# Kernel tuning notes

Measured on AMD Instinct MI355X. Metric: run time of the kernel, lower is better.

Reference implementation:

```python
import jax, jax.numpy as jnp
import numpy as np

B, S, D = 2, 2048, 1024
H = 16
HD = D // H  # 64


def setup_inputs() -> dict:
    key = jax.random.key(0)
    ks = jax.random.split(key, 6)
    sc = 1.0 / np.sqrt(D)
    x = jax.random.normal(ks[0], (B, S, D), dtype=jnp.float32)
    Wq = jax.random.normal(ks[1], (D, D), dtype=jnp.float32) * sc
    Wk = jax.random.normal(ks[2], (D, D), dtype=jnp.float32) * sc
    Wv = jax.random.normal(ks[3], (D, D), dtype=jnp.float32) * sc
    Wo = jax.random.normal(ks[4], (D, D), dtype=jnp.float32) * sc
    bo = jax.random.normal(ks[5], (D,), dtype=jnp.float32) * 0.01
    return {"x": x, "Wq": Wq, "Wk": Wk, "Wv": Wv, "Wo": Wo, "bo": bo}


def reference(x, Wq, Wk, Wv, Wo, bo):
    # projections: [B,S,D] -> [B,H,S,HD]
    def split_heads(t):
        return t.reshape(B, S, H, HD).transpose(0, 2, 1, 3)

    q = split_heads(x @ Wq)
    k = split_heads(x @ Wk)
    v = split_heads(x @ Wv)

    # naive full score matrix [B,H,S,S], masked causal, scaled softmax
    scores = jnp.einsum("bhqd,bhkd->bhqk", q, k)
    causal = jnp.tril(jnp.ones((S, S), dtype=bool))  # True = keep
    scores = jnp.where(causal, scores, -jnp.inf)
    attn = jax.nn.softmax(scores / np.sqrt(HD), axis=-1)

    ctx = jnp.einsum("bhqk,bhkd->bhqd", attn, v)  # [B,H,S,HD]
    ctx = ctx.transpose(0, 2, 1, 3).reshape(B, S, D)
    return ctx @ Wo + bo
```

## Files before the change

### kernel.cpp

```cpp
#include <hip/hip_runtime.h>

#define BB 2
#define SS 2048
#define DD 1024
#define HH 16
#define HD 64
#define MM (BB*SS)

typedef __bf16 bf16x8 __attribute__((ext_vector_type(8)));
typedef short  s16x4  __attribute__((ext_vector_type(4)));
typedef float  f32x4  __attribute__((ext_vector_type(4)));

#ifndef __has_builtin
#define __has_builtin(x) 0
#endif

__device__ __forceinline__ unsigned short f2bf(float f) {
    unsigned int u = __float_as_uint(f);
    u = (u + 0x7fffu + ((u >> 16) & 1u)) >> 16;
    return (unsigned short)u;
}
__device__ __forceinline__ unsigned int pack2(float a, float b) {
    return (unsigned int)f2bf(a) | ((unsigned int)f2bf(b) << 16);
}
__device__ __forceinline__ unsigned int pack2_fast(float a, float b) {
#if __has_builtin(__builtin_amdgcn_perm)
    return __builtin_amdgcn_perm(__float_as_uint(b) + 0x8000u,
                                 __float_as_uint(a) + 0x8000u, 0x07060302u);
#else
    return ((__float_as_uint(a) + 0x8000u) >> 16) |
           ((__float_as_uint(b) + 0x8000u) & 0xffff0000u);
#endif
}

__device__ __forceinline__ void gload_lds16(const unsigned short* g, unsigned short* l) {
    __builtin_amdgcn_global_load_lds(
        (const __attribute__((address_space(1))) void*)g,
        (__attribute__((address_space(3))) void*)l, 16, 0, 0);
}

__global__ __launch_bounds__(256) void prep_kernel(const float* __restrict__ x,
                                                   const float* __restrict__ Wq,
                                                   const float* __restrict__ Wk,
                                                   const float* __restrict__ Wv,
                                                   const float* __restrict__ Wo,
                                                   unsigned short* __restrict__ Xb,
                                                   unsigned short* __restrict__ Wqkvt,
                                                   unsigned short* __restrict__ Wot) {
    __shared__ float tile[32][33];
    const int bx = blockIdx.x;
    const int t = threadIdx.x;
    if (bx < 2048) {
        int gid = bx * 256 + t;
        int i = gid * 8;
        float4 a = *(const float4*)(x + i);
        float4 b = *(const float4*)(x + i + 4);
        uint4 o;
        o.x = pack2(a.x, a.y); o.y = pack2(a.z, a.w);
        o.z = pack2(b.x, b.y); o.w = pack2(b.z, b.w);
        ((uint4*)Xb)[gid] = o;
        return;
    }
    int pb = bx - 2048;
    int p = pb >> 10, rem = pb & 1023;
    int bxx = rem & 31, byy = rem >> 5;
    const float* src = (p == 0) ? Wq : (p == 1) ? Wk : (p == 2) ? Wv : Wo;
    unsigned short* dst = (p == 3) ? Wot : (Wqkvt + (size_t)p * DD * DD);
    int tx = t & 31, ty = t >> 5;
    int n = bxx * 32 + tx;
#pragma unroll
    for (int i = 0; i < 4; ++i) {
        int k = byy * 32 + ty + i * 8;
        tile[ty + i * 8][tx] = src[k * DD + n];
    }
    __syncthreads();
#pragma unroll
    for (int i = 0; i < 4; ++i) {
        int n2 = bxx * 32 + ty + i * 8;
        int k2 = byy * 32 + tx;
        dst[n2 * DD + k2] = f2bf(tile[tx][ty + i * 8]);
    }
}

#define GEMM_K_LOOP(Aglob, Bglob)                                                 \
    __shared__ unsigned short smem[128 * 132];                                    \
    unsigned short (*As)[64]  = (unsigned short(*)[64])smem;                      \
    unsigned short (*Bs)[64]  = (unsigned short(*)[64])(smem + 128 * 64);         \
    unsigned short (*Es)[132] = (unsigned short(*)[132])smem;                     \
    const int n0 = blockIdx.x * 128, m0 = blockIdx.y * 128;                       \
    const int t = threadIdx.x;                                                    \
    const int wave = t >> 6, lane = t & 63;                                       \
    const int wm = wave >> 1, wn = wave & 1;                                      \
    const int l15 = lane & 15, quad = lane >> 4;                                  \
    const int lr = lane >> 3, lg = (lane & 7);                                    \
    const int lc = (lg ^ lr) * 8;                    \
    f32x4 acc[4][4];                                                              \
    _Pragma("unroll") for (int i = 0; i < 4; ++i)                                 \
        _Pragma("unroll") for (int j = 0; j < 4; ++j) acc[i][j] = f32x4{0,0,0,0}; \
    for (int kt = 0; kt < 16; ++kt) {                                             \
        if (kt) __syncthreads();                                                  \
        _Pragma("unroll") for (int i = 0; i < 4; ++i) {                           \
            int row = wave * 32 + i * 8;                                          \
            gload_lds16(Aglob + (size_t)(m0 + row + lr) * DD + kt * 64 + lc, &As[row][0]); \
            gload_lds16(Bglob + (size_t)(n0 + row + lr) * DD + kt * 64 + lc, &Bs[row][0]); \
        }                                                                         \
        __syncthreads();                                                          \
        _Pragma("unroll") for (int kh = 0; kh < 2; ++kh) {                        \
            bf16x8 af[4], bfr[4];                                                 \
            _Pragma("unroll") for (int s = 0; s < 4; ++s)                         \
                af[s] = *(const bf16x8*)&As[wm * 64 + s * 16 + l15][((kh * 4 + quad) ^ (l15 & 7)) * 8]; \
            _Pragma("unroll") for (int s = 0; s < 4; ++s)                         \
                bfr[s] = *(const bf16x8*)&Bs[wn * 64 + s * 16 + l15][((kh * 4 + quad) ^ (l15 & 7)) * 8]; \
            _Pragma("unroll") for (int i = 0; i < 4; ++i)                         \
                _Pragma("unroll") for (int j = 0; j < 4; ++j)                     \
                    acc[i][j] = __builtin_amdgcn_mfma_f32_16x16x32_bf16(af[i], bfr[j], acc[i][j], 0, 0, 0); \
        }                                                                         \
    }                                                                             \
    __syncthreads();

__global__ __launch_bounds__(256) void qkv_gemm_kernel(const unsigned short* __restrict__ Xb,
                                                       const unsigned short* __restrict__ Wt,
                                                       unsigned short* __restrict__ Qg,
                                                       unsigned short* __restrict__ Kg,
                                                       unsigned short* __restrict__ Vt) {
    GEMM_K_LOOP(Xb, Wt)
    const int p = n0 >> 10;
    const float qs = (p == 0) ? 0.18033688011112042f : 1.0f;
    if (p < 2) {
#pragma unroll
        for (int sm = 0; sm < 4; ++sm)
#pragma unroll
            for (int sn = 0; sn < 4; ++sn)
#pragma unroll
                for (int i = 0; i < 4; ++i)
                    Es[wm * 64 + sm * 16 + quad * 4 + i][wn * 64 + sn * 16 + l15] = f2bf(acc[sm][sn][i] * qs);
    } else {
#pragma unroll
        for (int sm = 0; sm < 4; ++sm)
#pragma unroll
            for (int sn = 0; sn < 4; ++sn)
#pragma unroll
                for (int i = 0; i < 4; ++i)
                    Es[wn * 64 + sn * 16 + l15][wm * 64 + sm * 16 + quad * 4 + i] = f2bf(acc[sm][sn][i]);
    }
    __syncthreads();
    const int h0 = (n0 & 1023) >> 6;
    if (p < 2) {
        unsigned short* dst0 = p ? Kg : Qg;
        int ml = t >> 1, seg = t & 1;
        int gm = m0 + ml, b = gm >> 11, s = gm & 2047;
        unsigned short* dptr = dst0 + ((size_t)(b * HH + h0 + seg) * SS + s) * HD;
#pragma unroll
        for (int j = 0; j < 8; ++j)
            *(uint4*)(dptr + j * 8) = *(const uint4*)&Es[ml][seg * 64 + j * 8];
    } else {
        int nl = t >> 1, mh = t & 1;
        int h = h0 + (nl >> 6), hd = nl & 63;
        int b = m0 >> 11, s0 = (m0 & 2047) + mh * 64;
        unsigned short* dptr = Vt + ((size_t)(b * HH + h) * HD + hd) * SS + s0;
#pragma unroll
        for (int j = 0; j < 8; ++j)
            *(uint4*)(dptr + j * 8) = *(const uint4*)&Es[nl][mh * 64 + j * 8];
    }
}

__global__ __launch_bounds__(256) void out_gemm_kernel(const unsigned short* __restrict__ Ctxb,
                                                       const unsigned short* __restrict__ Wot,
                                                       const float* __restrict__ bo,
                                                       float* __restrict__ out) {
    GEMM_K_LOOP(Ctxb, Wot)
    (void)Es;
#pragma unroll
    for (int sn = 0; sn < 4; ++sn) {
        int gn = n0 + wn * 64 + sn * 16 + l15;
        float bias = bo[gn];
#pragma unroll
        for (int sm = 0; sm < 4; ++sm)
#pragma unroll
            for (int i = 0; i < 4; ++i) {
                int gm = m0 + wm * 64 + sm * 16 + quad * 4 + i;
                out[(size_t)gm * DD + gn] = acc[sm][sn][i] + bias;
            }
    }
}

__global__ __launch_bounds__(256) void attn_kernel(const unsigned short* __restrict__ Qg,
                                                   const unsigned short* __restrict__ Kg,
                                                   const unsigned short* __restrict__ Vt,
                                                   unsigned short* __restrict__ Ctxb) {
    __shared__ unsigned short Ks[2][128][64];
    __shared__ unsigned short Vs[2][64][128];

    const int bh = blockIdx.x;
    const int pi = blockIdx.y;
    const int t = threadIdx.x;
    const int wave = t >> 6, lane = t & 63;
    const int l15 = lane & 15, quad = lane >> 4;
    const int q0A = pi * 64;
    const int q0B = (31 - pi) * 64;
    const int aIters = (pi + 2) >> 1;
    const int bIters = (33 - pi) >> 1;
    const int b = bh >> 4, h = bh & 15;

    const unsigned short* Qb = Qg + (size_t)bh * SS * HD;
    const unsigned short* Kb = Kg + (size_t)bh * SS * HD;
    const unsigned short* Vb = Vt + (size_t)bh * HD * SS;

    const int qrow0 = q0A + wave * 16 + l15;
    const int qrow1 = q0B + wave * 16 + l15;
    const int qA_hi = q0A + wave * 16 + 15;
    const int qB_hi = q0B + wave * 16 + 15;
    bf16x8 bq[2][2];
#pragma unroll
    for (int hh = 0; hh < 2; ++hh) {
        bq[0][hh] = *(const bf16x8*)(Qb + (size_t)qrow0 * HD + hh * 32 + quad * 8);
        bq[1][hh] = *(const bf16x8*)(Qb + (size_t)qrow1 * HD + hh * 32 + quad * 8);
    }

    const int rloc = lane >> 3, pcl = lane & 7;
    const int vrl = lane >> 4, vgc = lane & 15;
    const unsigned short* ksrc[4];
    const unsigned short* vsrc[4];
#pragma unroll
    for (int j = 0; j < 4; ++j) {
        int krow = (wave * 4 + j) * 8 + rloc;
        ksrc[j] = Kb + (size_t)krow * HD + (pcl ^ rloc) * 8;
        int vrow = wave * 16 + j * 4 + vrl;
        vsrc[j] = Vb + (size_t)vrow * SS + (vgc ^ (vrow & 15)) * 8;
    }

    f32x4 acc[2][4];
#pragma unroll
    for (int qf = 0; qf < 2; ++qf)
#pragma unroll
        for (int db = 0; db < 4; ++db) acc[qf][db] = f32x4{0,0,0,0};
    f32x4 accl[2] = {f32x4{0,0,0,0}, f32x4{0,0,0,0}};
    const s16x4 ones = {(short)0x3F80, (short)0x3F80, (short)0x3F80, (short)0x3F80};

#pragma unroll
    for (int j = 0; j < 4; ++j) {
        gload_lds16(ksrc[j], &Ks[0][(wave * 4 + j) * 8][0]);
        gload_lds16(vsrc[j], &Vs[0][wave * 16 + j * 4][0]);
    }
    __syncthreads();

    for (int kt = 0; kt < bIters; ++kt) {
        const int buf = kt & 1;
        const int k0 = kt * 128;
        if (kt + 1 < bIters) {
            const int nb = buf ^ 1;
#pragma unroll
            for (int j = 0; j < 4; ++j) {
                gload_lds16(ksrc[j] + (size_t)(kt + 1) * 128 * HD, &Ks[nb][(wave * 4 + j) * 8][0]);
                gload_lds16(vsrc[j] + (kt + 1) * 128,              &Vs[nb][wave * 16 + j * 4][0]);
            }
        }

        const bool diagA = (kt == aIters - 1);
        const bool diagB = (kt == bIters - 1);
        const bool inA = (kt < aIters);
#pragma unroll
        for (int kb = 0; kb < 8; ++kb) {
            const int kbase = k0 + kb * 16;
            const bool a0 = inA && (kbase <= qA_hi);
            const bool a1 = (kbase <= qB_hi);
            if (!a0 && !a1) continue;
            bf16x8 ak[2];
#pragma unroll
            for (int hh = 0; hh < 2; ++hh)
                ak[hh] = *(const bf16x8*)&Ks[buf][kb * 16 + l15][((hh * 4 + quad) ^ (l15 & 7)) * 8];

            f32x4 St[2] = {f32x4{0,0,0,0}, f32x4{0,0,0,0}};
            if (a0) {
#pragma unroll
                for (int hh = 0; hh < 2; ++hh)
                    St[0] = __builtin_amdgcn_mfma_f32_16x16x32_bf16(ak[hh], bq[0][hh], St[0], 0, 0, 0);
                if (diagA) {
#pragma unroll
                    for (int r = 0; r < 4; ++r)
                        if (kbase + quad * 4 + r > qrow0) St[0][r] = -1e30f;
                }
            }
            if (a1) {
#pragma unroll
                for (int hh = 0; hh < 2; ++hh)
                    St[1] = __builtin_amdgcn_mfma_f32_16x16x32_bf16(ak[hh], bq[1][hh], St[1], 0, 0, 0);
                if (diagB) {
#pragma unroll
                    for (int r = 0; r < 4; ++r)
                        if (kbase + quad * 4 + r > qrow1) St[1][r] = -1e30f;
                }
            }

            s16x4 ap[2];
#pragma unroll
            for (int qf = 0; qf < 2; ++qf) {
                float e0 = __builtin_amdgcn_exp2f(St[qf][0]);
                float e1 = __builtin_amdgcn_exp2f(St[qf][1]);
                float e2 = __builtin_amdgcn_exp2f(St[qf][2]);
                float e3 = __builtin_amdgcn_exp2f(St[qf][3]);
                uint2 uu;
                uu.x = pack2_fast(e0, e1);
                uu.y = pack2_fast(e2, e3);
                ap[qf] = *(s16x4*)&uu;
            }

#pragma unroll
            for (int db = 0; db < 4; ++db) {
                const int pg = (2 * kb + (quad >> 1)) ^ l15;
                s16x4 bv = *(const s16x4*)&Vs[buf][db * 16 + l15][pg * 8 + (quad & 1) * 4];
                if (a0) acc[0][db] = __builtin_amdgcn_mfma_f32_16x16x16bf16_1k(ap[0], bv, acc[0][db], 0, 0, 0);
                if (a1) acc[1][db] = __builtin_amdgcn_mfma_f32_16x16x16bf16_1k(ap[1], bv, acc[1][db], 0, 0, 0);
            }
            if (a0) accl[0] = __builtin_amdgcn_mfma_f32_16x16x16bf16_1k(ap[0], ones, accl[0], 0, 0, 0);
            if (a1) accl[1] = __builtin_amdgcn_mfma_f32_16x16x16bf16_1k(ap[1], ones, accl[1], 0, 0, 0);
        }

        __syncthreads();
    }

#pragma unroll
    for (int qf = 0; qf < 2; ++qf) {
        const int qb0 = (qf == 0) ? q0A : q0B;
#pragma unroll
        for (int r = 0; r < 4; ++r) {
            float ir = 1.0f / accl[qf][r];
            int gq = qb0 + wave * 16 + quad * 4 + r;
            size_t base = ((size_t)(b * SS + gq)) * DD + h * HD;
#pragma unroll
            for (int db = 0; db < 4; ++db)
                Ctxb[base + db * 16 + l15] = f2bf(acc[qf][db][r] * ir);
        }
    }
}

extern "C" void kernel_launch(void* const* d_in, const int* in_sizes, int n_in,
                              void* d_out, int out_size, void* d_ws, size_t ws_size,
                              hipStream_t stream) {
    const float* x  = (const float*)d_in[0];
    const float* Wq = (const float*)d_in[1];
    const float* Wk = (const float*)d_in[2];
    const float* Wv = (const float*)d_in[3];
    const float* Wo = (const float*)d_in[4];
    const float* bo = (const float*)d_in[5];
    float* out = (float*)d_out;

    char* w = (char*)d_ws;
    unsigned short* Xb    = (unsigned short*)(w);
    unsigned short* Wqkvt = (unsigned short*)(w + (size_t)(8 << 20));
    unsigned short* Wot   = (unsigned short*)(w + (size_t)(14 << 20));
    unsigned short* Qg    = (unsigned short*)(w + (size_t)(16 << 20));
    unsigned short* Kg    = (unsigned short*)(w + (size_t)(24 << 20));
    unsigned short* Vt    = (unsigned short*)(w + (size_t)(32 << 20));
    unsigned short* Ctxb  = (unsigned short*)(w + (size_t)(40 << 20));

    prep_kernel<<<6144, 256, 0, stream>>>(x, Wq, Wk, Wv, Wo, Xb, Wqkvt, Wot);
    qkv_gemm_kernel<<<dim3(3 * DD / 128, MM / 128), 256, 0, stream>>>(Xb, Wqkvt, Qg, Kg, Vt);
    attn_kernel<<<dim3(BB * HH, 16), 256, 0, stream>>>(Qg, Kg, Vt, Ctxb);
    out_gemm_kernel<<<dim3(DD / 128, MM / 128), 256, 0, stream>>>(Ctxb, Wot, bo, out);
}
```

Baseline: 207.2 us.

## Split causal attention loop into paired and tail phases; widen weight-transpose tiles

The attention kernel's single key-tile loop, which evaluated per-16-key predicates for both query blocks, becomes two loops. The first covers tiles both query blocks need and runs unconditionally, masking only the diagonal. The second covers only the long query block's remaining tiles, removing branch and predicate overhead from the inner MFMA loop. The prep kernel's weight transpose moves from 32x32 to 64x64 tiles with 16-byte packed bf16 stores and half the blocks, trading possible LDS bank conflicts on the strided reads for fewer, wider global writes.

Result: faster. 174.8 us (-15.6%).

```diff
diff --git a/kernel.cpp b/kernel.cpp
--- a/kernel.cpp
+++ b/kernel.cpp
@@ -47,7 +47,7 @@
                                                    unsigned short* __restrict__ Xb,
                                                    unsigned short* __restrict__ Wqkvt,
                                                    unsigned short* __restrict__ Wot) {
-    __shared__ float tile[32][33];
+    __shared__ float tile[64][65];
     const int bx = blockIdx.x;
     const int t = threadIdx.x;
     if (bx < 2048) {
@@ -62,24 +62,30 @@
         return;
     }
     int pb = bx - 2048;
-    int p = pb >> 10, rem = pb & 1023;
-    int bxx = rem & 31, byy = rem >> 5;
+    int p = pb >> 8, rem = pb & 255;
+    int tn = rem & 15, tk = rem >> 4;
     const float* src = (p == 0) ? Wq : (p == 1) ? Wk : (p == 2) ? Wv : Wo;
     unsigned short* dst = (p == 3) ? Wot : (Wqkvt + (size_t)p * DD * DD);
-    int tx = t & 31, ty = t >> 5;
-    int n = bxx * 32 + tx;
-#pragma unroll
-    for (int i = 0; i < 4; ++i) {
-        int k = byy * 32 + ty + i * 8;
-        tile[ty + i * 8][tx] = src[k * DD + n];
+    const int nn = t & 63, kk0 = t >> 6;
+#pragma unroll
+    for (int i = 0; i < 16; ++i) {
+        int kk = kk0 + i * 4;
+        tile[kk][nn] = src[(size_t)(tk * 64 + kk) * DD + tn * 64 + nn];
     }
     __syncthreads();
-#pragma unroll
-    for (int i = 0; i < 4; ++i) {
-        int n2 = bxx * 32 + ty + i * 8;
-        int k2 = byy * 32 + tx;
-        dst[n2 * DD + k2] = f2bf(tile[tx][ty + i * 8]);
-    }
+    const int nrow = t >> 2, kc = (t & 3) * 16;
+    uint4 o0, o1;
+    o0.x = pack2(tile[kc + 0][nrow],  tile[kc + 1][nrow]);
+    o0.y = pack2(tile[kc + 2][nrow],  tile[kc + 3][nrow]);
+    o0.z = pack2(tile[kc + 4][nrow],  tile[kc + 5][nrow]);
+    o0.w = pack2(tile[kc + 6][nrow],  tile[kc + 7][nrow]);
+    o1.x = pack2(tile[kc + 8][nrow],  tile[kc + 9][nrow]);
+    o1.y = pack2(tile[kc + 10][nrow], tile[kc + 11][nrow]);
+    o1.z = pack2(tile[kc + 12][nrow], tile[kc + 13][nrow]);
+    o1.w = pack2(tile[kc + 14][nrow], tile[kc + 15][nrow]);
+    unsigned short* dptr = dst + (size_t)(tn * 64 + nrow) * DD + tk * 64 + kc;
+    *(uint4*)(dptr) = o0;
+    *(uint4*)(dptr + 8) = o1;
 }
 
 #define GEMM_K_LOOP(Aglob, Bglob)                                                 \
@@ -208,8 +214,6 @@
 
     const int qrow0 = q0A + wave * 16 + l15;
     const int qrow1 = q0B + wave * 16 + l15;
-    const int qA_hi = q0A + wave * 16 + 15;
-    const int qB_hi = q0B + wave * 16 + 15;
     bf16x8 bq[2][2];
 #pragma unroll
     for (int hh = 0; hh < 2; ++hh) {
@@ -244,7 +248,7 @@
     }
     __syncthreads();
 
-    for (int kt = 0; kt < bIters; ++kt) {
+    for (int kt = 0; kt < aIters; ++kt) {
         const int buf = kt & 1;
         const int k0 = kt * 128;
         if (kt + 1 < bIters) {
@@ -255,43 +259,25 @@
                 gload_lds16(vsrc[j] + (kt + 1) * 128,              &Vs[nb][wave * 16 + j * 4][0]);
             }
         }
-
         const bool diagA = (kt == aIters - 1);
-        const bool diagB = (kt == bIters - 1);
-        const bool inA = (kt < aIters);
 #pragma unroll
         for (int kb = 0; kb < 8; ++kb) {
             const int kbase = k0 + kb * 16;
-            const bool a0 = inA && (kbase <= qA_hi);
-            const bool a1 = (kbase <= qB_hi);
-            if (!a0 && !a1) continue;
             bf16x8 ak[2];
 #pragma unroll
             for (int hh = 0; hh < 2; ++hh)
                 ak[hh] = *(const bf16x8*)&Ks[buf][kb * 16 + l15][((hh * 4 + quad) ^ (l15 & 7)) * 8];
-
             f32x4 St[2] = {f32x4{0,0,0,0}, f32x4{0,0,0,0}};
-            if (a0) {
-#pragma unroll
-                for (int hh = 0; hh < 2; ++hh)
-                    St[0] = __builtin_amdgcn_mfma_f32_16x16x32_bf16(ak[hh], bq[0][hh], St[0], 0, 0, 0);
-                if (diagA) {
-#pragma unroll
-                    for (int r = 0; r < 4; ++r)
-                        if (kbase + quad * 4 + r > qrow0) St[0][r] = -1e30f;
-                }
-            }
-            if (a1) {
-#pragma unroll
-                for (int hh = 0; hh < 2; ++hh)
-                    St[1] = __builtin_amdgcn_mfma_f32_16x16x32_bf16(ak[hh], bq[1][hh], St[1], 0, 0, 0);
-                if (diagB) {
-#pragma unroll
-                    for (int r = 0; r < 4; ++r)
-                        if (kbase + quad * 4 + r > qrow1) St[1][r] = -1e30f;
-                }
-            }
-
+#pragma unroll
+            for (int hh = 0; hh < 2; ++hh) {
+                St[0] = __builtin_amdgcn_mfma_f32_16x16x32_bf16(ak[hh], bq[0][hh], St[0], 0, 0, 0);
+                St[1] = __builtin_amdgcn_mfma_f32_16x16x32_bf16(ak[hh], bq[1][hh], St[1], 0, 0, 0);
+            }
+            if (diagA) {
+#pragma unroll
+                for (int r = 0; r < 4; ++r)
+                    if (kbase + quad * 4 + r > qrow0) St[0][r] = -1e30f;
+            }
             s16x4 ap[2];
 #pragma unroll
             for (int qf = 0; qf < 2; ++qf) {
@@ -304,18 +290,61 @@
                 uu.y = pack2_fast(e2, e3);
                 ap[qf] = *(s16x4*)&uu;
             }
-
 #pragma unroll
             for (int db = 0; db < 4; ++db) {
                 const int pg = (2 * kb + (quad >> 1)) ^ l15;
                 s16x4 bv = *(const s16x4*)&Vs[buf][db * 16 + l15][pg * 8 + (quad & 1) * 4];
-                if (a0) acc[0][db] = __builtin_amdgcn_mfma_f32_16x16x16bf16_1k(ap[0], bv, acc[0][db], 0, 0, 0);
-                if (a1) acc[1][db] = __builtin_amdgcn_mfma_f32_16x16x16bf16_1k(ap[1], bv, acc[1][db], 0, 0, 0);
-            }
-            if (a0) accl[0] = __builtin_amdgcn_mfma_f32_16x16x16bf16_1k(ap[0], ones, accl[0], 0, 0, 0);
-            if (a1) accl[1] = __builtin_amdgcn_mfma_f32_16x16x16bf16_1k(ap[1], ones, accl[1], 0, 0, 0);
-        }
-
+                acc[0][db] = __builtin_amdgcn_mfma_f32_16x16x16bf16_1k(ap[0], bv, acc[0][db], 0, 0, 0);
+                acc[1][db] = __builtin_amdgcn_mfma_f32_16x16x16bf16_1k(ap[1], bv, acc[1][db], 0, 0, 0);
+            }
+            accl[0] = __builtin_amdgcn_mfma_f32_16x16x16bf16_1k(ap[0], ones, accl[0], 0, 0, 0);
+            accl[1] = __builtin_amdgcn_mfma_f32_16x16x16bf16_1k(ap[1], ones, accl[1], 0, 0, 0);
+        }
+        __syncthreads();
+    }
+
+    for (int kt = aIters; kt < bIters; ++kt) {
+        const int buf = kt & 1;
+        const int k0 = kt * 128;
+        if (kt + 1 < bIters) {
+            const int nb = buf ^ 1;
+#pragma unroll
+            for (int j = 0; j < 4; ++j) {
+                gload_lds16(ksrc[j] + (size_t)(kt + 1) * 128 * HD, &Ks[nb][(wave * 4 + j) * 8][0]);
+                gload_lds16(vsrc[j] + (kt + 1) * 128,              &Vs[nb][wave * 16 + j * 4][0]);
+            }
+        }
+        const bool diagB = (kt == bIters - 1);
+#pragma unroll
+        for (int kb = 0; kb < 8; ++kb) {
+            const int kbase = k0 + kb * 16;
+            f32x4 St = f32x4{0, 0, 0, 0};
+#pragma unroll
+            for (int hh = 0; hh < 2; ++hh) {
+                bf16x8 ak = *(const bf16x8*)&Ks[buf][kb * 16 + l15][((hh * 4 + quad) ^ (l15 & 7)) * 8];
+                St = __builtin_amdgcn_mfma_f32_16x16x32_bf16(ak, bq[1][hh], St, 0, 0, 0);
+            }
+            if (diagB) {
+#pragma unroll
+                for (int r = 0; r < 4; ++r)
+                    if (kbase + quad * 4 + r > qrow1) St[r] = -1e30f;
+            }
+            float e0 = __builtin_amdgcn_exp2f(St[0]);
+            float e1 = __builtin_amdgcn_exp2f(St[1]);
+            float e2 = __builtin_amdgcn_exp2f(St[2]);
+            float e3 = __builtin_amdgcn_exp2f(St[3]);
+            uint2 uu;
+            uu.x = pack2_fast(e0, e1);
+            uu.y = pack2_fast(e2, e3);
+            s16x4 ap = *(s16x4*)&uu;
+#pragma unroll
+            for (int db = 0; db < 4; ++db) {
+                const int pg = (2 * kb + (quad >> 1)) ^ l15;
+                s16x4 bv = *(const s16x4*)&Vs[buf][db * 16 + l15][pg * 8 + (quad & 1) * 4];
+                acc[1][db] = __builtin_amdgcn_mfma_f32_16x16x16bf16_1k(ap, bv, acc[1][db], 0, 0, 0);
+            }
+            accl[1] = __builtin_amdgcn_mfma_f32_16x16x16bf16_1k(ap, ones, accl[1], 0, 0, 0);
+        }
         __syncthreads();
     }
 
@@ -354,7 +383,7 @@
     unsigned short* Vt    = (unsigned short*)(w + (size_t)(32 << 20));
     unsigned short* Ctxb  = (unsigned short*)(w + (size_t)(40 << 20));
 
-    prep_kernel<<<6144, 256, 0, stream>>>(x, Wq, Wk, Wv, Wo, Xb, Wqkvt, Wot);
+    prep_kernel<<<3072, 256, 0, stream>>>(x, Wq, Wk, Wv, Wo, Xb, Wqkvt, Wot);
     qkv_gemm_kernel<<<dim3(3 * DD / 128, MM / 128), 256, 0, stream>>>(Xb, Wqkvt, Qg, Kg, Vt);
     attn_kernel<<<dim3(BB * HH, 16), 256, 0, stream>>>(Qg, Kg, Vt, Ctxb);
     out_gemm_kernel<<<dim3(DD / 128, MM / 128), 256, 0, stream>>>(Ctxb, Wot, bo, out);
```
